# Performance work log

Measured on AMD Instinct MI355X. Metric: run time of the kernel, lower is better.

The kernel has to match this reference:

```python
import jax, jax.numpy as jnp
import numpy as np

EPS = 1e-5

def _layernorm(x, g, b):
    mu = jnp.mean(x, axis=-1, keepdims=True)
    var = jnp.mean(jnp.square(x - mu), axis=-1, keepdims=True)
    return (x - mu) * jax.lax.rsqrt(var + EPS) * g + b

def setup_inputs() -> dict:
    key = jax.random.key(0)
    ks = jax.random.split(key, 4)
    E, B, D, H = 8, 131072, 128, 128
    features = jax.random.normal(ks[0], (E, B, D), dtype=jnp.float32)
    gate_w1 = jax.random.normal(ks[1], (E * D, H), dtype=jnp.float32) * (1.0 / np.sqrt(E * D))
    gate_b1 = jnp.zeros((H,), dtype=jnp.float32)
    ln1_g = jnp.ones((H,), dtype=jnp.float32)
    ln1_b = jnp.zeros((H,), dtype=jnp.float32)
    gate_w2 = jax.random.normal(ks[2], (H, E), dtype=jnp.float32) * (1.0 / np.sqrt(H))
    gate_b2 = jnp.zeros((E,), dtype=jnp.float32)
    out_g = jnp.ones((D,), dtype=jnp.float32)
    out_b = jnp.zeros((D,), dtype=jnp.float32)
    return {"features": features, "gate_w1": gate_w1, "gate_b1": gate_b1,
            "ln1_g": ln1_g, "ln1_b": ln1_b, "gate_w2": gate_w2, "gate_b2": gate_b2,
            "out_g": out_g, "out_b": out_b}

def reference(features, gate_w1, gate_b1, ln1_g, ln1_b, gate_w2, gate_b2, out_g, out_b):
    # features: [E, B, D]
    E, B, D = features.shape
    # concat teacher features per sample -> [B, E*D]
    concat = jnp.transpose(features, (1, 0, 2)).reshape(B, E * D)
    h = concat @ gate_w1 + gate_b1                       # [B, 128]
    h = jax.nn.gelu(h, approximate=False)                # torch nn.GELU default = exact
    h = _layernorm(h, ln1_g, ln1_b)
    logits = h @ gate_w2 + gate_b2                       # [B, E]
    scores = jax.nn.softmax(logits, axis=-1)             # [B, E]
    # per-expert scalar weight then LayerNorm over D
    weighted = scores.T[:, :, None] * features           # [E, B, D]
    out = _layernorm(weighted, out_g, out_b)             # [E, B, D]
    return out
```

## Files before the change

### kernel.cpp

```cpp
#include <hip/hip_runtime.h>
#include <hip/hip_bf16.h>

#define B_N   131072
#define E_N   8
#define D_N   128
#define H_N   128
#define K_N   1024
#define MBLK  16
#define NTHR  256

typedef __attribute__((ext_vector_type(8))) short bf16x8;
typedef __attribute__((ext_vector_type(4))) float f32x4;
typedef __attribute__((ext_vector_type(4))) unsigned short u16x4;

__device__ __forceinline__ unsigned short f2bf(float f) {
    union { float f; unsigned int i; } c; c.f = f;
    unsigned int x = c.i;
    return (unsigned short)((x + 0x7fffu + ((x >> 16) & 1u)) >> 16);
}
__device__ __forceinline__ float bf2f(unsigned short u) {
    union { unsigned int i; float f; } c; c.i = ((unsigned int)u) << 16; return c.f;
}

__global__ void prep_w1_frags(const float* __restrict__ w1,
                              unsigned short* __restrict__ frag) {
    int t    = blockIdx.x * blockDim.x + threadIdx.x;
    int lane = t & 63;
    int fgi  = t >> 6;
    int kst  = fgi >> 3;
    int nt   = fgi & 7;
    int n    = nt * 16 + (lane & 15);
    int k0   = kst * 32 + (lane >> 4) * 8;
    bf16x8 v;
    #pragma unroll
    for (int j = 0; j < 8; ++j)
        v[j] = (short)f2bf(w1[(k0 + j) * H_N + n]);
    *reinterpret_cast<bf16x8*>(frag + (size_t)t * 8) = v;
}

__global__ __launch_bounds__(NTHR, 3)
void moe_fused(const float* __restrict__ feats,
               const unsigned short* __restrict__ w1frag,
               const float* __restrict__ gate_b1,
               const float* __restrict__ ln1_g,
               const float* __restrict__ ln1_b,
               const float* __restrict__ gate_w2,
               const float* __restrict__ gate_b2,
               const float* __restrict__ out_g,
               const float* __restrict__ out_b,
               float* __restrict__ out)
{
    __shared__ __attribute__((aligned(16))) unsigned short featS[MBLK * K_N];
    __shared__ float hS[MBLK * 132];
    __shared__ float w2tS[E_N * H_N];
    __shared__ float gb1S[H_N], l1gS[H_N], l1bS[H_N], ogS[D_N], obS[D_N];
    __shared__ float gb2S[E_N];
    __shared__ float scoreS[MBLK * E_N];

    const int tid = threadIdx.x;
    const int b0  = blockIdx.x * MBLK;

    if (tid < 128) {
        gb1S[tid] = gate_b1[tid];
        l1gS[tid] = ln1_g[tid];
        l1bS[tid] = ln1_b[tid];
        ogS[tid]  = out_g[tid];
        obS[tid]  = out_b[tid];
    }
    if (tid < 8) gb2S[tid] = gate_b2[tid];
    for (int idx = tid; idx < H_N * E_N; idx += NTHR)
        w2tS[(idx & 7) * H_N + (idx >> 3)] = gate_w2[idx];

    #pragma unroll
    for (int e = 0; e < E_N; ++e) {
        const f32x4* src = reinterpret_cast<const f32x4*>(
            feats + ((size_t)e * B_N + b0) * D_N);
        #pragma unroll
        for (int i = 0; i < (MBLK * D_N / 4) / NTHR; ++i) {
            int f   = tid + i * NTHR;
            f32x4 v = src[f];
            int m   = f >> 5;
            int dq  = f & 31;
            int k   = e * D_N + dq * 4;
            int uoff = m * K_N + ((((k >> 3) ^ (m & 7)) << 3) | (k & 7));
            u16x4 u;
            u[0] = f2bf(v[0]); u[1] = f2bf(v[1]);
            u[2] = f2bf(v[2]); u[3] = f2bf(v[3]);
            *reinterpret_cast<u16x4*>(&featS[uoff]) = u;
        }
    }
    __syncthreads();

    const int wv   = tid >> 6;
    const int lane = tid & 63;
    const int lrow = lane & 15;
    const int lkh  = lane >> 4;
    const int nt0  = wv * 2, nt1 = nt0 + 1;
    f32x4 acc0 = {0.f, 0.f, 0.f, 0.f};
    f32x4 acc1 = {0.f, 0.f, 0.f, 0.f};
    const bf16x8* wf = reinterpret_cast<const bf16x8*>(w1frag);
    const int arow = lrow * K_N;
    const int asw  = lrow & 7;
    #pragma unroll 4
    for (int kk = 0; kk < 32; ++kk) {
        bf16x8 a  = *reinterpret_cast<const bf16x8*>(
            &featS[arow + ((((kk << 2) + lkh) ^ asw) << 3)]);
        bf16x8 b0 = wf[((kk * 8 + nt0) << 6) + lane];
        bf16x8 b1 = wf[((kk * 8 + nt1) << 6) + lane];
        acc0 = __builtin_amdgcn_mfma_f32_16x16x32_bf16(a, b0, acc0, 0, 0, 0);
        acc1 = __builtin_amdgcn_mfma_f32_16x16x32_bf16(a, b1, acc1, 0, 0, 0);
    }

    {
        const int colA = nt0 * 16 + lrow;
        const int colB = nt1 * 16 + lrow;
        #pragma unroll
        for (int r = 0; r < 4; ++r) {
            int row  = lkh * 4 + r;
            float vA = acc0[r] + gb1S[colA];
            float vB = acc1[r] + gb1S[colB];
            vA = 0.5f * vA * (1.f + erff(vA * 0.70710678118654752f));
            vB = 0.5f * vB * (1.f + erff(vB * 0.70710678118654752f));
            hS[row * 132 + colA] = vA;
            hS[row * 132 + colB] = vB;
        }
    }
    __syncthreads();

    {
        const int row = tid >> 4;
        const int gl  = tid & 15;
        const float* hrow = &hS[row * 132 + gl * 8];
        float hv[8];
        #pragma unroll
        for (int j = 0; j < 8; ++j) hv[j] = hrow[j];
        float s = 0.f, sq = 0.f;
        #pragma unroll
        for (int j = 0; j < 8; ++j) { s += hv[j]; sq += hv[j] * hv[j]; }
        #pragma unroll
        for (int msk = 1; msk < 16; msk <<= 1) {
            s  += __shfl_xor(s, msk);
            sq += __shfl_xor(sq, msk);
        }
        float mu  = s * (1.f / 128.f);
        float var = sq * (1.f / 128.f) - mu * mu;
        float rs  = rsqrtf(var + 1e-5f);
        float p[8] = {0.f, 0.f, 0.f, 0.f, 0.f, 0.f, 0.f, 0.f};
        #pragma unroll
        for (int j = 0; j < 8; ++j) {
            int col  = gl * 8 + j;
            float hn = (hv[j] - mu) * rs * l1gS[col] + l1bS[col];
            #pragma unroll
            for (int e = 0; e < 8; ++e) p[e] += hn * w2tS[e * H_N + col];
        }
        #pragma unroll
        for (int msk = 1; msk < 16; msk <<= 1) {
            #pragma unroll
            for (int e = 0; e < 8; ++e) p[e] += __shfl_xor(p[e], msk);
        }
        float lg[8], mx = -3.0e38f;
        #pragma unroll
        for (int e = 0; e < 8; ++e) { lg[e] = p[e] + gb2S[e]; mx = fmaxf(mx, lg[e]); }
        float den = 0.f, ex[8];
        #pragma unroll
        for (int e = 0; e < 8; ++e) { ex[e] = __expf(lg[e] - mx); den += ex[e]; }
        float inv = 1.f / den;
        if (gl < 8) scoreS[row * 8 + gl] = ex[gl] * inv;
    }
    __syncthreads();

    {
        const int m  = tid >> 4;
        const int gl = tid & 15;
        #pragma unroll
        for (int e = 0; e < E_N; ++e) {
            int slot = ((e << 4) | gl) ^ (m & 7);
            bf16x8 x8 = *reinterpret_cast<const bf16x8*>(&featS[m * K_N + (slot << 3)]);
            float x[8];
            #pragma unroll
            for (int j = 0; j < 8; ++j) x[j] = bf2f((unsigned short)x8[j]);
            float s = 0.f, sq = 0.f;
            #pragma unroll
            for (int j = 0; j < 8; ++j) { s += x[j]; sq += x[j] * x[j]; }
            #pragma unroll
            for (int msk = 1; msk < 16; msk <<= 1) {
                s  += __shfl_xor(s, msk);
                sq += __shfl_xor(sq, msk);
            }
            float mu  = s * (1.f / 128.f);
            float var = sq * (1.f / 128.f) - mu * mu;
            float sc  = scoreS[m * 8 + e];
            float srs = sc * rsqrtf(sc * sc * var + 1e-5f);
            float* dst = out + ((size_t)e * B_N + b0 + m) * D_N + gl * 8;
            f32x4 o0, o1;
            #pragma unroll
            for (int j = 0; j < 4; ++j)
                o0[j] = (x[j] - mu) * srs * ogS[gl * 8 + j] + obS[gl * 8 + j];
            #pragma unroll
            for (int j = 0; j < 4; ++j)
                o1[j] = (x[4 + j] - mu) * srs * ogS[gl * 8 + 4 + j] + obS[gl * 8 + 4 + j];
            *reinterpret_cast<f32x4*>(dst)     = o0;
            *reinterpret_cast<f32x4*>(dst + 4) = o1;
        }
    }
}

extern "C" void kernel_launch(void* const* d_in, const int* in_sizes, int n_in,
                              void* d_out, int out_size, void* d_ws, size_t ws_size,
                              hipStream_t stream) {
    const float* feats   = (const float*)d_in[0];
    const float* gate_w1 = (const float*)d_in[1];
    const float* gate_b1 = (const float*)d_in[2];
    const float* ln1_g   = (const float*)d_in[3];
    const float* ln1_b   = (const float*)d_in[4];
    const float* gate_w2 = (const float*)d_in[5];
    const float* gate_b2 = (const float*)d_in[6];
    const float* out_g   = (const float*)d_in[7];
    const float* out_b   = (const float*)d_in[8];
    float* outp = (float*)d_out;
    unsigned short* frag = (unsigned short*)d_ws;

    prep_w1_frags<<<64, NTHR, 0, stream>>>(gate_w1, frag);
    moe_fused<<<B_N / MBLK, NTHR, 0, stream>>>(
        feats, frag, gate_b1, ln1_g, ln1_b, gate_w2, gate_b2, out_g, out_b, outp);
}
```

Before: 301.5 us.

## Make fused MoE gate kernel persistent with register-resident W1 and prefetching

```diff
diff --git a/kernel.cpp b/kernel.cpp
--- a/kernel.cpp
+++ b/kernel.cpp
@@ -7,11 +7,13 @@
 #define H_N   128
 #define K_N   1024
 #define MBLK  16
-#define NTHR  256
+#define NTHR  1024
+#define GRID  1024
+#define TPB   ((B_N / MBLK) / GRID)
 
 typedef __attribute__((ext_vector_type(8))) short bf16x8;
 typedef __attribute__((ext_vector_type(4))) float f32x4;
-typedef __attribute__((ext_vector_type(4))) unsigned short u16x4;
+typedef __attribute__((ext_vector_type(8))) unsigned short u16x8;
 
 __device__ __forceinline__ unsigned short f2bf(float f) {
     union { float f; unsigned int i; } c; c.f = f;
@@ -20,6 +22,13 @@
 }
 __device__ __forceinline__ float bf2f(unsigned short u) {
     union { unsigned int i; float f; } c; c.i = ((unsigned int)u) << 16; return c.f;
+}
+
+__device__ __forceinline__ void lds_barrier() {
+    __builtin_amdgcn_sched_barrier(0);
+    asm volatile("s_waitcnt lgkmcnt(0)" ::: "memory");
+    __builtin_amdgcn_s_barrier();
+    __builtin_amdgcn_sched_barrier(0);
 }
 
 __global__ void prep_w1_frags(const float* __restrict__ w1,
@@ -38,7 +47,7 @@
     *reinterpret_cast<bf16x8*>(frag + (size_t)t * 8) = v;
 }
 
-__global__ __launch_bounds__(NTHR, 3)
+__global__ __launch_bounds__(NTHR, 4)
 void moe_fused(const float* __restrict__ feats,
                const unsigned short* __restrict__ w1frag,
                const float* __restrict__ gate_b1,
@@ -50,157 +59,184 @@
                const float* __restrict__ out_b,
                float* __restrict__ out)
 {
-    __shared__ __attribute__((aligned(16))) unsigned short featS[MBLK * K_N];
-    __shared__ float hS[MBLK * 132];
-    __shared__ float w2tS[E_N * H_N];
-    __shared__ float gb1S[H_N], l1gS[H_N], l1bS[H_N], ogS[D_N], obS[D_N];
-    __shared__ float gb2S[E_N];
-    __shared__ float scoreS[MBLK * E_N];
-
-    const int tid = threadIdx.x;
-    const int b0  = blockIdx.x * MBLK;
-
-    if (tid < 128) {
-        gb1S[tid] = gate_b1[tid];
-        l1gS[tid] = ln1_g[tid];
-        l1bS[tid] = ln1_b[tid];
-        ogS[tid]  = out_g[tid];
-        obS[tid]  = out_b[tid];
+    __shared__ __attribute__((aligned(16))) unsigned short featS[2][MBLK * K_N];
+    __shared__ __attribute__((aligned(16))) unsigned short hSb[MBLK * 136];
+    __shared__ __attribute__((aligned(16))) float redS[8 * 64 * 4];
+    __shared__ __attribute__((aligned(16))) float w2S[H_N * E_N];
+    __shared__ float gb1S[128], l1gS[128], l1bS[128], ogS[128], obS[128], gb2S[8];
+    __shared__ float statSum[MBLK * 8], statSq[MBLK * 8], muS[MBLK * 8], srsS[MBLK * 8];
+
+    const int tid  = threadIdx.x;
+    const int bid  = blockIdx.x;
+    const int lane = tid & 63;
+    const int m    = tid >> 6;
+    const int sub  = tid & 63;
+    const int ee   = sub >> 3;
+    const int cc   = sub & 7;
+    const int sw   = m & 7;
+
+    const int kg = m >> 3;
+    const int ng = m & 7;
+    const int r_ = lane & 15;
+    const int kh = lane >> 4;
+
+    if (tid < 256)       reinterpret_cast<f32x4*>(w2S)[tid] = reinterpret_cast<const f32x4*>(gate_w2)[tid];
+    else if (tid < 384)  gb1S[tid - 256] = gate_b1[tid - 256];
+    else if (tid < 512)  l1gS[tid - 384] = ln1_g[tid - 384];
+    else if (tid < 640)  l1bS[tid - 512] = ln1_b[tid - 512];
+    else if (tid < 768)  ogS[tid - 640]  = out_g[tid - 640];
+    else if (tid < 896)  obS[tid - 768]  = out_b[tid - 768];
+    else if (tid < 904)  gb2S[tid - 896] = gate_b2[tid - 896];
+
+    const bf16x8* wf = reinterpret_cast<const bf16x8*>(w1frag);
+    bf16x8 wfr[16];
+    #pragma unroll
+    for (int i = 0; i < 16; ++i)
+        wfr[i] = wf[(((kg * 16 + i) * 8 + ng) << 6) + lane];
+
+    f32x4 pv[4];
+    {
+        const float* base = feats + ((size_t)ee * B_N + (size_t)bid * TPB * MBLK + m) * D_N + cc * 16;
+        #pragma unroll
+        for (int j = 0; j < 4; ++j) pv[j] = reinterpret_cast<const f32x4*>(base)[j];
     }
-    if (tid < 8) gb2S[tid] = gate_b2[tid];
-    for (int idx = tid; idx < H_N * E_N; idx += NTHR)
-        w2tS[(idx & 7) * H_N + (idx >> 3)] = gate_w2[idx];
-
-    #pragma unroll
-    for (int e = 0; e < E_N; ++e) {
-        const f32x4* src = reinterpret_cast<const f32x4*>(
-            feats + ((size_t)e * B_N + b0) * D_N);
-        #pragma unroll
-        for (int i = 0; i < (MBLK * D_N / 4) / NTHR; ++i) {
-            int f   = tid + i * NTHR;
-            f32x4 v = src[f];
-            int m   = f >> 5;
-            int dq  = f & 31;
-            int k   = e * D_N + dq * 4;
-            int uoff = m * K_N + ((((k >> 3) ^ (m & 7)) << 3) | (k & 7));
-            u16x4 u;
-            u[0] = f2bf(v[0]); u[1] = f2bf(v[1]);
-            u[2] = f2bf(v[2]); u[3] = f2bf(v[3]);
-            *reinterpret_cast<u16x4*>(&featS[uoff]) = u;
-        }
-    }
-    __syncthreads();
-
-    const int wv   = tid >> 6;
-    const int lane = tid & 63;
-    const int lrow = lane & 15;
-    const int lkh  = lane >> 4;
-    const int nt0  = wv * 2, nt1 = nt0 + 1;
-    f32x4 acc0 = {0.f, 0.f, 0.f, 0.f};
-    f32x4 acc1 = {0.f, 0.f, 0.f, 0.f};
-    const bf16x8* wf = reinterpret_cast<const bf16x8*>(w1frag);
-    const int arow = lrow * K_N;
-    const int asw  = lrow & 7;
-    #pragma unroll 4
-    for (int kk = 0; kk < 32; ++kk) {
-        bf16x8 a  = *reinterpret_cast<const bf16x8*>(
-            &featS[arow + ((((kk << 2) + lkh) ^ asw) << 3)]);
-        bf16x8 b0 = wf[((kk * 8 + nt0) << 6) + lane];
-        bf16x8 b1 = wf[((kk * 8 + nt1) << 6) + lane];
-        acc0 = __builtin_amdgcn_mfma_f32_16x16x32_bf16(a, b0, acc0, 0, 0, 0);
-        acc1 = __builtin_amdgcn_mfma_f32_16x16x32_bf16(a, b1, acc1, 0, 0, 0);
-    }
-
-    {
-        const int colA = nt0 * 16 + lrow;
-        const int colB = nt1 * 16 + lrow;
-        #pragma unroll
-        for (int r = 0; r < 4; ++r) {
-            int row  = lkh * 4 + r;
-            float vA = acc0[r] + gb1S[colA];
-            float vB = acc1[r] + gb1S[colB];
-            vA = 0.5f * vA * (1.f + erff(vA * 0.70710678118654752f));
-            vB = 0.5f * vB * (1.f + erff(vB * 0.70710678118654752f));
-            hS[row * 132 + colA] = vA;
-            hS[row * 132 + colB] = vB;
-        }
-    }
-    __syncthreads();
-
-    {
-        const int row = tid >> 4;
-        const int gl  = tid & 15;
-        const float* hrow = &hS[row * 132 + gl * 8];
-        float hv[8];
-        #pragma unroll
-        for (int j = 0; j < 8; ++j) hv[j] = hrow[j];
-        float s = 0.f, sq = 0.f;
-        #pragma unroll
-        for (int j = 0; j < 8; ++j) { s += hv[j]; sq += hv[j] * hv[j]; }
-        #pragma unroll
-        for (int msk = 1; msk < 16; msk <<= 1) {
-            s  += __shfl_xor(s, msk);
-            sq += __shfl_xor(sq, msk);
-        }
-        float mu  = s * (1.f / 128.f);
-        float var = sq * (1.f / 128.f) - mu * mu;
-        float rs  = rsqrtf(var + 1e-5f);
-        float p[8] = {0.f, 0.f, 0.f, 0.f, 0.f, 0.f, 0.f, 0.f};
-        #pragma unroll
-        for (int j = 0; j < 8; ++j) {
-            int col  = gl * 8 + j;
-            float hn = (hv[j] - mu) * rs * l1gS[col] + l1bS[col];
-            #pragma unroll
-            for (int e = 0; e < 8; ++e) p[e] += hn * w2tS[e * H_N + col];
-        }
-        #pragma unroll
-        for (int msk = 1; msk < 16; msk <<= 1) {
-            #pragma unroll
-            for (int e = 0; e < 8; ++e) p[e] += __shfl_xor(p[e], msk);
-        }
-        float lg[8], mx = -3.0e38f;
-        #pragma unroll
-        for (int e = 0; e < 8; ++e) { lg[e] = p[e] + gb2S[e]; mx = fmaxf(mx, lg[e]); }
-        float den = 0.f, ex[8];
-        #pragma unroll
-        for (int e = 0; e < 8; ++e) { ex[e] = __expf(lg[e] - mx); den += ex[e]; }
-        float inv = 1.f / den;
-        if (gl < 8) scoreS[row * 8 + gl] = ex[gl] * inv;
-    }
-    __syncthreads();
-
-    {
-        const int m  = tid >> 4;
-        const int gl = tid & 15;
-        #pragma unroll
-        for (int e = 0; e < E_N; ++e) {
-            int slot = ((e << 4) | gl) ^ (m & 7);
-            bf16x8 x8 = *reinterpret_cast<const bf16x8*>(&featS[m * K_N + (slot << 3)]);
-            float x[8];
-            #pragma unroll
-            for (int j = 0; j < 8; ++j) x[j] = bf2f((unsigned short)x8[j]);
+
+    for (int g = 0; g < TPB; ++g) {
+        const size_t b0 = (size_t)(bid * TPB + g) * MBLK;
+        unsigned short* fS = featS[g & 1];
+
+        {
             float s = 0.f, sq = 0.f;
-            #pragma unroll
-            for (int j = 0; j < 8; ++j) { s += x[j]; sq += x[j] * x[j]; }
-            #pragma unroll
-            for (int msk = 1; msk < 16; msk <<= 1) {
-                s  += __shfl_xor(s, msk);
-                sq += __shfl_xor(sq, msk);
-            }
-            float mu  = s * (1.f / 128.f);
-            float var = sq * (1.f / 128.f) - mu * mu;
-            float sc  = scoreS[m * 8 + e];
-            float srs = sc * rsqrtf(sc * sc * var + 1e-5f);
-            float* dst = out + ((size_t)e * B_N + b0 + m) * D_N + gl * 8;
-            f32x4 o0, o1;
-            #pragma unroll
-            for (int j = 0; j < 4; ++j)
-                o0[j] = (x[j] - mu) * srs * ogS[gl * 8 + j] + obS[gl * 8 + j];
-            #pragma unroll
-            for (int j = 0; j < 4; ++j)
-                o1[j] = (x[4 + j] - mu) * srs * ogS[gl * 8 + 4 + j] + obS[gl * 8 + 4 + j];
-            *reinterpret_cast<f32x4*>(dst)     = o0;
-            *reinterpret_cast<f32x4*>(dst + 4) = o1;
+            u16x8 ua, ub;
+            #pragma unroll
+            for (int t2 = 0; t2 < 16; ++t2) {
+                float v = pv[t2 >> 2][t2 & 3];
+                unsigned short u = f2bf(v);
+                float x = bf2f(u);
+                s += x; sq += x * x;
+                if (t2 < 8) ua[t2] = u; else ub[t2 - 8] = u;
+            }
+            s  += __shfl_xor(s, 1);  sq += __shfl_xor(sq, 1);
+            s  += __shfl_xor(s, 2);  sq += __shfl_xor(sq, 2);
+            s  += __shfl_xor(s, 4);  sq += __shfl_xor(sq, 4);
+            if (cc == 0) { statSum[m * 8 + ee] = s; statSq[m * 8 + ee] = sq; }
+            const int kb0 = ee * 16 + cc * 2;
+            *reinterpret_cast<u16x8*>(&fS[m * K_N + (((kb0)     ^ sw) << 3)]) = ua;
+            *reinterpret_cast<u16x8*>(&fS[m * K_N + (((kb0 + 1) ^ sw) << 3)]) = ub;
+        }
+
+        if (g + 1 < TPB) {
+            const float* basen = feats + ((size_t)ee * B_N + b0 + MBLK + m) * D_N + cc * 16;
+            #pragma unroll
+            for (int j = 0; j < 4; ++j) pv[j] = reinterpret_cast<const f32x4*>(basen)[j];
+        }
+
+        lds_barrier();
+
+        f32x4 acc = {0.f, 0.f, 0.f, 0.f};
+        {
+            const int abase = r_ * K_N;
+            #pragma unroll
+            for (int i = 0; i < 16; ++i) {
+                const int slot = (((kg * 16 + i) << 2) + kh) ^ (r_ & 7);
+                bf16x8 a = *reinterpret_cast<const bf16x8*>(&fS[abase + (slot << 3)]);
+                acc = __builtin_amdgcn_mfma_f32_16x16x32_bf16(a, wfr[i], acc, 0, 0, 0);
+            }
+        }
+        if (kg == 1)
+            *reinterpret_cast<f32x4*>(&redS[(ng * 64 + lane) * 4]) = acc;
+
+        lds_barrier();
+
+        if (kg == 0) {
+            f32x4 o = *reinterpret_cast<const f32x4*>(&redS[(ng * 64 + lane) * 4]);
+            const int col = ng * 16 + r_;
+            const float gb = gb1S[col];
+            #pragma unroll
+            for (int r2 = 0; r2 < 4; ++r2) {
+                float v = acc[r2] + o[r2] + gb;
+                v = 0.5f * v * (1.f + erff(v * 0.70710678118654752f));
+                hSb[(kh * 4 + r2) * 136 + col] = f2bf(v);
+            }
+        }
+
+        lds_barrier();
+
+        {
+            const int c0 = lane * 2;
+            unsigned int hh = *reinterpret_cast<const unsigned int*>(&hSb[m * 136 + c0]);
+            float h0 = bf2f((unsigned short)(hh & 0xffffu));
+            float h1 = bf2f((unsigned short)(hh >> 16));
+            float s2 = h0 + h1, q2 = h0 * h0 + h1 * h1;
+            #pragma unroll
+            for (int msk = 1; msk < 64; msk <<= 1) {
+                s2 += __shfl_xor(s2, msk);
+                q2 += __shfl_xor(q2, msk);
+            }
+            float mu  = s2 * (1.f / 128.f);
+            float var = q2 * (1.f / 128.f) - mu * mu;
+            float rs  = rsqrtf(var + 1e-5f);
+            float hn0 = (h0 - mu) * rs * l1gS[c0]     + l1bS[c0];
+            float hn1 = (h1 - mu) * rs * l1gS[c0 + 1] + l1bS[c0 + 1];
+            f32x4 wa0 = *reinterpret_cast<const f32x4*>(&w2S[c0 * 8]);
+            f32x4 wb0 = *reinterpret_cast<const f32x4*>(&w2S[c0 * 8 + 4]);
+            f32x4 wa1 = *reinterpret_cast<const f32x4*>(&w2S[(c0 + 1) * 8]);
+            f32x4 wb1 = *reinterpret_cast<const f32x4*>(&w2S[(c0 + 1) * 8 + 4]);
+            float p[8];
+            #pragma unroll
+            for (int e = 0; e < 4; ++e) {
+                p[e]     = hn0 * wa0[e] + hn1 * wa1[e];
+                p[e + 4] = hn0 * wb0[e] + hn1 * wb1[e];
+            }
+            #pragma unroll
+            for (int msk = 1; msk < 64; msk <<= 1) {
+                #pragma unroll
+                for (int e = 0; e < 8; ++e) p[e] += __shfl_xor(p[e], msk);
+            }
+            float mx = -3.0e38f;
+            #pragma unroll
+            for (int e = 0; e < 8; ++e) { p[e] += gb2S[e]; mx = fmaxf(mx, p[e]); }
+            float den = 0.f;
+            #pragma unroll
+            for (int e = 0; e < 8; ++e) { p[e] = __expf(p[e] - mx); den += p[e]; }
+            const float inv = 1.f / den;
+            if (lane < 8) {
+                float pe = p[0];
+                #pragma unroll
+                for (int e = 1; e < 8; ++e) pe = (lane == e) ? p[e] : pe;
+                float sc   = pe * inv;
+                float ss   = statSum[m * 8 + lane], qq = statSq[m * 8 + lane];
+                float mu2  = ss * (1.f / 128.f);
+                float var2 = qq * (1.f / 128.f) - mu2 * mu2;
+                muS[m * 8 + lane]  = mu2;
+                srsS[m * 8 + lane] = sc * rsqrtf(sc * sc * var2 + 1e-5f);
+            }
+        }
+
+        lds_barrier();
+
+        {
+            const int kb0 = ee * 16 + cc * 2;
+            bf16x8 xa = *reinterpret_cast<const bf16x8*>(&fS[m * K_N + (((kb0)     ^ sw) << 3)]);
+            bf16x8 xb = *reinterpret_cast<const bf16x8*>(&fS[m * K_N + (((kb0 + 1) ^ sw) << 3)]);
+            const float mu  = muS[m * 8 + ee];
+            const float srs = srsS[m * 8 + ee];
+            float* dst = out + ((size_t)ee * B_N + b0 + m) * D_N + cc * 16;
+            const f32x4* ogv = reinterpret_cast<const f32x4*>(&ogS[cc * 16]);
+            const f32x4* obv = reinterpret_cast<const f32x4*>(&obS[cc * 16]);
+            #pragma unroll
+            for (int j = 0; j < 4; ++j) {
+                f32x4 og = ogv[j], ob = obv[j];
+                f32x4 o;
+                #pragma unroll
+                for (int q = 0; q < 4; ++q) {
+                    int idx = j * 4 + q;
+                    unsigned short u = (idx < 8) ? (unsigned short)xa[idx]
+                                                 : (unsigned short)xb[idx - 8];
+                    o[q] = (bf2f(u) - mu) * srs * og[q] + ob[q];
+                }
+                reinterpret_cast<f32x4*>(dst)[j] = o;
+            }
         }
     }
 }
@@ -220,7 +256,7 @@
     float* outp = (float*)d_out;
     unsigned short* frag = (unsigned short*)d_ws;
 
-    prep_w1_frags<<<64, NTHR, 0, stream>>>(gate_w1, frag);
-    moe_fused<<<B_N / MBLK, NTHR, 0, stream>>>(
+    prep_w1_frags<<<64, 256, 0, stream>>>(gate_w1, frag);
+    moe_fused<<<GRID, NTHR, 0, stream>>>(
         feats, frag, gate_b1, ln1_g, ln1_b, gate_w2, gate_b2, out_g, out_b, outp);
 }
```

Result: slower. 664.6 us (+120.4%).
